# Performance work log

Measured on AMD Instinct MI355X. Metric: run time of the kernel, lower is better.

Reference implementation:

```python
import jax, jax.numpy as jnp
import numpy as np

B, T, F = 2048, 96, 32
H = 1024
G_EMB = 16
LSTM_IN = F + 11 + 1 + G_EMB  # 60


def _lstm_cell(x, h, c, W_ih, W_hh, b):
    g = x @ W_ih.T + h @ W_hh.T + b
    i, f, gg, o = jnp.split(g, 4, axis=-1)  # torch gate order: i, f, g, o
    c_new = jax.nn.sigmoid(f) * c + jax.nn.sigmoid(i) * jnp.tanh(gg)
    h_new = jax.nn.sigmoid(o) * jnp.tanh(c_new)
    return h_new, c_new


def setup_inputs() -> dict:
    key = jax.random.key(0)
    ks = jax.random.split(key, 26)
    s = 1.0 / np.sqrt(H)
    inp = {
        "dec_known": jax.random.normal(ks[0], (B, T, F), jnp.float32),
        "target_y": jax.random.normal(ks[1], (B, T, 1), jnp.float32),
        "enc_h": jax.random.normal(ks[2], (2, B, H), jnp.float32),
        "enc_c": jax.random.normal(ks[3], (2, B, H), jnp.float32),
        "last_enc_consumption": jax.random.normal(ks[4], (B, 1), jnp.float32),
        "group_ids": jax.random.randint(ks[5], (B,), 0, 1000),
        "cat_province": jax.random.randint(ks[6], (B,), 0, 13),
        "cat_customer_type": jax.random.randint(ks[7], (B,), 0, 2),
        "cat_price_type": jax.random.randint(ks[8], (B,), 0, 5),
        "cat_consumption_level": jax.random.randint(ks[9], (B,), 0, 3),
        # learned parameters
        "group_emb": jax.random.normal(ks[10], (1000, G_EMB), jnp.float32),
        "emb_province": jax.random.normal(ks[11], (13, 4), jnp.float32),
        "emb_customer_type": jax.random.normal(ks[12], (2, 2), jnp.float32),
        "emb_price_type": jax.random.normal(ks[13], (5, 3), jnp.float32),
        "emb_consumption_level": jax.random.normal(ks[14], (3, 2), jnp.float32),
        "W_ih0": jax.random.normal(ks[15], (4 * H, LSTM_IN), jnp.float32) * s,
        "W_hh0": jax.random.normal(ks[16], (4 * H, H), jnp.float32) * s,
        "b0": jax.random.normal(ks[17], (4 * H,), jnp.float32) * s,
        "W_ih1": jax.random.normal(ks[18], (4 * H, H), jnp.float32) * s,
        "W_hh1": jax.random.normal(ks[19], (4 * H, H), jnp.float32) * s,
        "b1": jax.random.normal(ks[20], (4 * H,), jnp.float32) * s,
        "W_proj": jax.random.normal(ks[21], (1, H), jnp.float32) * s,
        "b_proj": jnp.zeros((1,), jnp.float32),
    }
    return inp


def reference(dec_known, target_y, enc_h, enc_c, last_enc_consumption,
              group_ids, cat_province, cat_customer_type, cat_price_type,
              cat_consumption_level, group_emb, emb_province, emb_customer_type,
              emb_price_type, emb_consumption_level, W_ih0, W_hh0, b0,
              W_ih1, W_hh1, b1, W_proj, b_proj):
    b, t, _ = dec_known.shape
    # static per-sample features (categorical + group embeddings)
    cat_emb = jnp.concatenate([
        emb_province[cat_province], emb_customer_type[cat_customer_type],
        emb_price_type[cat_price_type], emb_consumption_level[cat_consumption_level],
    ], axis=-1)  # [B, 11]
    group_vec = group_emb[group_ids]  # [B, 16]
    static = jnp.concatenate([cat_emb, group_vec], axis=-1)  # [B, 27]
    # teacher_forcing_ratio = 1.0 => prev_y is last_enc_consumption then target_y shifted
    prev_y = jnp.concatenate([last_enc_consumption[:, None, :], target_y[:, :-1, :]], axis=1)  # [B,T,1]
    x = jnp.concatenate([
        prev_y, dec_known,
        jnp.broadcast_to(static[:, None, :], (b, t, static.shape[-1])),
    ], axis=-1)  # [B, T, 60]

    def step(carry, x_t):
        h1, c1, h2, c2 = carry
        h1, c1 = _lstm_cell(x_t, h1, c1, W_ih0, W_hh0, b0)
        h2, c2 = _lstm_cell(h1, h2, c2, W_ih1, W_hh1, b1)
        return (h1, c1, h2, c2), h2

    init = (enc_h[0], enc_c[0], enc_h[1], enc_c[1])
    _, hs = jax.lax.scan(step, init, jnp.swapaxes(x, 0, 1))  # hs: [T, B, H]
    y = jnp.einsum('tbh,oh->bto', hs, W_proj) + b_proj  # [B, T, 1]
    return y
```

## Files before the change

### kernel.cpp

```cpp
#include <hip/hip_runtime.h>
#include <hip/hip_bf16.h>
#include <stdint.h>


#define BB  2048
#define TT  96
#define NG  4096
#define NT0 34
#define NT1 64

typedef __bf16 bf16;
typedef __bf16 bf16x8 __attribute__((ext_vector_type(8)));
typedef float  f32x4  __attribute__((ext_vector_type(4)));

__device__ __forceinline__ float sigm(float x) { return 1.0f / (1.0f + __expf(-x)); }
__device__ __forceinline__ float ftanh(float x) { return 2.0f / (1.0f + __expf(-2.0f * x)) - 1.0f; }

__device__ __forceinline__ void gload16(const bf16* g, bf16* l) {
  __builtin_amdgcn_global_load_lds((const __attribute__((address_space(1))) void*)g,
                                   (__attribute__((address_space(3))) void*)l, 16, 0, 0);
}

#define SB()  __builtin_amdgcn_sched_barrier(0)
#define BAR() __builtin_amdgcn_s_barrier()


__global__ __launch_bounds__(256) void build_wf1(const float* __restrict__ Wih1,
                                                 const float* __restrict__ Whh1,
                                                 bf16* __restrict__ Wf) {
  int idx = blockIdx.x * 256 + threadIdx.x;
  if (idx >= 32 * NT1 * 4096) return;
  int j = idx & 7, lane = (idx >> 3) & 63, mw = (idx >> 9) & 3;
  int wg = (idx >> 11) & 1, kt = (idx >> 12) & 63, panel = idx >> 18;
  int np = panel * 128 + wg * 64 + mw * 16 + (lane & 15);
  int k  = kt * 32 + ((lane >> 4) << 3) + j;
  int n  = (np & 3) * 1024 + (np >> 2);
  float v = (k < 1024) ? Wih1[n * 1024 + k] : Whh1[n * 1024 + (k - 1024)];
  Wf[idx] = (bf16)v;
}

__global__ __launch_bounds__(256) void build_wf0(const float* __restrict__ Wih0,
                                                 const float* __restrict__ Whh0,
                                                 bf16* __restrict__ Wf) {
  int idx = blockIdx.x * 256 + threadIdx.x;
  if (idx >= 32 * NT0 * 4096) return;
  int j = idx & 7, lane = (idx >> 3) & 63, mw = (idx >> 9) & 3;
  int wg = (idx >> 11) & 1;
  int rem = idx >> 12;
  int kt = rem % NT0, panel = rem / NT0;
  int np = panel * 128 + wg * 64 + mw * 16 + (lane & 15);
  int k  = kt * 32 + ((lane >> 4) << 3) + j;
  int n  = (np & 3) * 1024 + (np >> 2);
  float v;
  if (k < 60)      v = Wih0[n * 60 + k];
  else if (k < 64) v = 0.0f;
  else             v = Whh0[n * 1024 + (k - 64)];
  Wf[idx] = (bf16)v;
}

__global__ __launch_bounds__(256) void perm_bias(const float* __restrict__ b0,
                                                 const float* __restrict__ b1,
                                                 float* __restrict__ b0p,
                                                 float* __restrict__ b1p) {
  int idx = blockIdx.x * 256 + threadIdx.x;
  if (idx >= NG) return;
  int n = (idx & 3) * 1024 + (idx >> 2);
  b0p[idx] = b0[n];
  b1p[idx] = b1[n];
}

__global__ __launch_bounds__(256) void build_x(
    const float* __restrict__ dec, const float* __restrict__ ty, const float* __restrict__ lec,
    const int* __restrict__ gid, const int* __restrict__ cp, const int* __restrict__ cct,
    const int* __restrict__ cpt, const int* __restrict__ ccl,
    const float* __restrict__ gemb, const float* __restrict__ ep, const float* __restrict__ ect,
    const float* __restrict__ ept, const float* __restrict__ ecl,
    bf16* __restrict__ X) {
  int idx = blockIdx.x * 256 + threadIdx.x;
  if (idx >= BB * TT) return;
  int b = idx / TT, t = idx % TT;
  bf16* x = X + (size_t)idx * 64;
  x[0] = (bf16)((t == 0) ? lec[b] : ty[b * TT + t - 1]);
  const float* d = dec + (size_t)idx * 32;
  #pragma unroll
  for (int k = 0; k < 32; ++k) x[1 + k] = (bf16)d[k];
  const float* e;
  e = ep  + cp[b]  * 4;  for (int j = 0; j < 4;  ++j) x[33 + j] = (bf16)e[j];
  e = ect + cct[b] * 2;  for (int j = 0; j < 2;  ++j) x[37 + j] = (bf16)e[j];
  e = ept + cpt[b] * 3;  for (int j = 0; j < 3;  ++j) x[39 + j] = (bf16)e[j];
  e = ecl + ccl[b] * 2;  for (int j = 0; j < 2;  ++j) x[42 + j] = (bf16)e[j];
  e = gemb + gid[b] * 16; for (int j = 0; j < 16; ++j) x[44 + j] = (bf16)e[j];
  for (int j = 60; j < 64; ++j) x[j] = (bf16)0.0f;
}

__global__ __launch_bounds__(256) void init_state(const float* __restrict__ enc_h,
                                                  const float* __restrict__ enc_c,
                                                  bf16* __restrict__ H1b,
                                                  bf16* __restrict__ H2b,
                                                  float* __restrict__ c1t,
                                                  float* __restrict__ c2t) {
  int idx = blockIdx.x * 256 + threadIdx.x;
  if (idx >= BB * 1024) return;
  int b = idx >> 10, h = idx & 1023;
  H1b[idx] = (bf16)enc_h[idx];
  H2b[idx] = (bf16)enc_h[(size_t)BB * 1024 + idx];
  c1t[(size_t)h * BB + b] = enc_c[idx];
  c2t[(size_t)h * BB + b] = enc_c[(size_t)BB * 1024 + idx];
}


template <int MODE>
__device__ __forceinline__ void body(
    int tm, int tn, int t,
    const bf16* __restrict__ P0, const bf16* __restrict__ P1,
    const bf16* __restrict__ Wf, const float* __restrict__ bperm,
    float* __restrict__ ct, bf16* __restrict__ Hout,
    const float* __restrict__ wp, const float* __restrict__ bp,
    float* __restrict__ y, bf16* As)
{
  constexpr int NT = MODE ? NT1 : NT0;

  const int tid = threadIdx.x;
  const int lane = tid & 63, w = tid >> 6;
  const int lrow = lane & 15, u = lane >> 4;
  const int wb = w & 1, wg = w >> 1;

  f32x4 acc[4][4];
  #pragma unroll
  for (int mw = 0; mw < 4; ++mw)
    #pragma unroll
    for (int nb = 0; nb < 4; ++nb) acc[mw][nb] = (f32x4){0.f, 0.f, 0.f, 0.f};

  const int r0 = tid >> 2, r1 = (256 + tid) >> 2;
  const int kc0 = (((tid & 3) ^ ((r0 >> 1) & 3)) << 3);
  const int kc1 = (((tid & 3) ^ ((r1 >> 1) & 3)) << 3);
  const int d0 = (tid & ~63) * 8;
  const int d1 = 2048 + d0;
  const int klocal = ((((lane >> 4) ^ (lrow >> 1)) & 3) << 3);

  auto aptr = [&](int row, int kt, int kc) -> const bf16* {
    if constexpr (MODE == 0) {
      return (kt < 2) ? (P0 + ((size_t)(tm + row) * TT + t) * 64 + kt * 32 + kc)
                      : (P1 + (size_t)(tm + row) * 1024 + (kt - 2) * 32 + kc);
    } else {
      return (kt < 32) ? (P0 + (size_t)(tm + row) * 1024 + kt * 32 + kc)
                       : (P1 + (size_t)(tm + row) * 1024 + (kt - 32) * 32 + kc);
    }
  };
  auto stageA = [&](int kt, bf16* buf) {
    gload16(aptr(r0, kt, kc0), buf + d0);
    gload16(aptr(r1, kt, kc1), buf + d1);
  };

  const bf16* wfbase = Wf + ((size_t)(tn >> 7) * NT) * 4096 + wg * 2048 + lane * 8;
  auto loadW = [&](bf16x8 (&wf)[4], int kt) {
    const bf16* p = wfbase + (size_t)kt * 4096;
    #pragma unroll
    for (int mw = 0; mw < 4; ++mw)
      wf[mw] = *reinterpret_cast<const bf16x8*>(p + mw * 512);
  };

  bf16x8 wfA[4], wfB[4];

  stageA(0, As);
  loadW(wfA, 0);
  stageA(1, As + 4096);
  asm volatile("s_waitcnt vmcnt(2)" ::: "memory");
  SB(); BAR(); SB();

  auto iter = [&](int kt, bf16x8 (&cur)[4], bf16x8 (&nxt)[4]) {
    bf16* buf = As + ((kt & 1) ? 4096 : 0);
    bf16x8 af[4];
    #pragma unroll
    for (int nb = 0; nb < 4; ++nb)
      af[nb] = *reinterpret_cast<const bf16x8*>(&buf[(wb * 64 + nb * 16 + lrow) * 32 + klocal]);
    asm volatile("s_waitcnt lgkmcnt(0)" ::: "memory");
    SB(); BAR(); SB();
    if (kt + 2 < NT) stageA(kt + 2, buf);
    if (kt + 1 < NT) loadW(nxt, kt + 1);
    SB();
    __builtin_amdgcn_s_setprio(1);
    #pragma unroll
    for (int mw = 0; mw < 4; ++mw)
      #pragma unroll
      for (int nb = 0; nb < 4; ++nb)
        acc[mw][nb] = __builtin_amdgcn_mfma_f32_16x16x32_bf16(cur[mw], af[nb], acc[mw][nb], 0, 0, 0);
    __builtin_amdgcn_s_setprio(0);
    if (kt + 2 < NT)      { asm volatile("s_waitcnt vmcnt(6)" ::: "memory"); }
    else if (kt + 1 < NT) { asm volatile("s_waitcnt vmcnt(4)" ::: "memory"); }
    else                  { asm volatile("s_waitcnt vmcnt(0)" ::: "memory"); }
    SB(); BAR(); SB();
  };

  for (int kt = 0; kt < NT; kt += 2) {
    iter(kt,     wfA, wfB);
    iter(kt + 1, wfB, wfA);
  }

  bf16* hst = As + w * 1024;
  const int hq = (tn >> 2) + wg * 16;
  const int bgb = tm + wb * 64;
  float yp[4] = {0.f, 0.f, 0.f, 0.f};

  #pragma unroll
  for (int mw = 0; mw < 4; ++mw) {
    int hg = hq + mw * 4 + u;
    f32x4 bv = *reinterpret_cast<const f32x4*>(&bperm[hg * 4]);
    float wph = 0.f;
    if constexpr (MODE == 1) wph = wp[hg];
    #pragma unroll
    for (int nb = 0; nb < 4; ++nb) {
      int bg = bgb + nb * 16 + lrow;
      float gi = acc[mw][nb][0] + bv[0];
      float gf = acc[mw][nb][1] + bv[1];
      float gg = acc[mw][nb][2] + bv[2];
      float go = acc[mw][nb][3] + bv[3];
      float* cp_ = ct + (size_t)hg * BB + bg;
      float c = *cp_;
      float cn = sigm(gf) * c + sigm(gi) * ftanh(gg);
      float hn = sigm(go) * ftanh(cn);
      *cp_ = cn;
      hst[(nb * 16 + lrow) * 16 + mw * 4 + u] = (bf16)hn;
      if constexpr (MODE == 1) yp[nb] += hn * wph;
    }
  }

  asm volatile("s_waitcnt lgkmcnt(0)" ::: "memory");
  SB();

  #pragma unroll
  for (int q = 0; q < 2; ++q) {
    int chunk = q * 64 + lane;
    int row = chunk >> 1, half = chunk & 1;
    bf16x8 v = *reinterpret_cast<const bf16x8*>(&hst[row * 16 + half * 8]);
    *reinterpret_cast<bf16x8*>(&Hout[(size_t)(bgb + row) * 1024 + hq + half * 8]) = v;
  }

  if constexpr (MODE == 1) {
    #pragma unroll
    for (int nb = 0; nb < 4; ++nb) {
      float s = yp[nb];
      s += __shfl_xor(s, 16);
      s += __shfl_xor(s, 32);
      if (lane < 16)
        atomicAdd(&y[(size_t)(bgb + nb * 16 + lane) * TT + t], s);
    }
  } else {
    if (tn == 0 && tid < 128) y[(size_t)(tm + tid) * TT + t] = bp[0];
  }
}

__global__ __launch_bounds__(256, 3) void step_kernel(
    const bf16* __restrict__ H1in, const bf16* __restrict__ H2in,
    bf16* __restrict__ H1out, bf16* __restrict__ H2out,
    const bf16* __restrict__ X,
    const bf16* __restrict__ Wf0, const bf16* __restrict__ Wf1,
    const float* __restrict__ b0p, const float* __restrict__ b1p,
    float* __restrict__ c1t, float* __restrict__ c2t,
    const float* __restrict__ wp, const float* __restrict__ bp,
    float* __restrict__ y, int t2, int only_l1) {
  __shared__ alignas(16) bf16 As[2 * 4096];
  int bid = (int)blockIdx.x;
  if (only_l1 || bid >= 512) {
    int v = only_l1 ? bid : bid - 512;
    int t1 = t2 + 1;
    if (t1 >= TT) return;
    int x = v & 7, j = v >> 3;
    int tm  = (j & 15) << 7;
    int tn0 = ((x << 1) + (j >> 4)) << 8;
    body<0>(tm, tn0, t1, X, H1in, Wf0, b0p, c1t, H1out, nullptr, bp, y, As);
    __syncthreads();
    body<0>(tm, tn0 + 128, t1, X, H1in, Wf0, b0p, c1t, H1out, nullptr, bp, y, As);
  } else {
    int x = bid & 7, j = bid >> 3;
    int tm = (j & 15) << 7;
    int tn = ((x << 2) + (j >> 4)) << 7;
    body<1>(tm, tn, t2, H1in, H2in, Wf1, b1p, c2t, H2out, wp, nullptr, y, As);
  }
}


extern "C" void kernel_launch(void* const* d_in, const int* in_sizes, int n_in,
                              void* d_out, int out_size, void* d_ws, size_t ws_size,
                              hipStream_t stream) {
  const float* dec   = (const float*)d_in[0];
  const float* ty    = (const float*)d_in[1];
  const float* enc_h = (const float*)d_in[2];
  const float* enc_c = (const float*)d_in[3];
  const float* lec   = (const float*)d_in[4];
  const int*   gid   = (const int*)d_in[5];
  const int*   cp    = (const int*)d_in[6];
  const int*   cct   = (const int*)d_in[7];
  const int*   cpt   = (const int*)d_in[8];
  const int*   ccl   = (const int*)d_in[9];
  const float* gemb  = (const float*)d_in[10];
  const float* ep    = (const float*)d_in[11];
  const float* ect   = (const float*)d_in[12];
  const float* ept   = (const float*)d_in[13];
  const float* ecl   = (const float*)d_in[14];
  const float* Wih0  = (const float*)d_in[15];
  const float* Whh0  = (const float*)d_in[16];
  const float* b0    = (const float*)d_in[17];
  const float* Wih1  = (const float*)d_in[18];
  const float* Whh1  = (const float*)d_in[19];
  const float* b1    = (const float*)d_in[20];
  const float* wp    = (const float*)d_in[21];
  const float* bp    = (const float*)d_in[22];
  float* y = (float*)d_out;

  char* ws = (char*)d_ws;
  bf16* Wf1   = (bf16*)ws;  ws += (size_t)32 * NT1 * 4096 * 2;
  bf16* Wf0   = (bf16*)ws;  ws += (size_t)32 * NT0 * 4096 * 2;
  bf16* X     = (bf16*)ws;  ws += (size_t)BB * TT * 64 * 2;
  bf16* H1a   = (bf16*)ws;  ws += (size_t)BB * 1024 * 2;
  bf16* H1b   = (bf16*)ws;  ws += (size_t)BB * 1024 * 2;
  bf16* H2a   = (bf16*)ws;  ws += (size_t)BB * 1024 * 2;
  bf16* H2b   = (bf16*)ws;  ws += (size_t)BB * 1024 * 2;
  float* c1t  = (float*)ws; ws += (size_t)BB * 1024 * 4;
  float* c2t  = (float*)ws; ws += (size_t)BB * 1024 * 4;
  float* b0p  = (float*)ws; ws += (size_t)NG * 4;
  float* b1p  = (float*)ws; ws += (size_t)NG * 4;

  build_wf1<<<(32 * NT1 * 4096) / 256, 256, 0, stream>>>(Wih1, Whh1, Wf1);
  build_wf0<<<(32 * NT0 * 4096 + 255) / 256, 256, 0, stream>>>(Wih0, Whh0, Wf0);
  perm_bias<<<NG / 256, 256, 0, stream>>>(b0, b1, b0p, b1p);
  build_x<<<(BB * TT + 255) / 256, 256, 0, stream>>>(dec, ty, lec, gid, cp, cct, cpt, ccl,
                                                     gemb, ep, ect, ept, ecl, X);
  init_state<<<(BB * 1024) / 256, 256, 0, stream>>>(enc_h, enc_c, H1b, H2b, c1t, c2t);

  step_kernel<<<256, 256, 0, stream>>>(H1b, nullptr, H1a, nullptr, X, Wf0, Wf1,
                                       b0p, b1p, c1t, c2t, wp, bp, y, -1, 1);
  for (int t = 0; t < TT; ++t) {
    bf16* h1i = (t & 1) ? H1b : H1a;
    bf16* h1o = (t & 1) ? H1a : H1b;
    bf16* h2i = (t & 1) ? H2a : H2b;
    bf16* h2o = (t & 1) ? H2b : H2a;
    step_kernel<<<768, 256, 0, stream>>>(h1i, h2i, h1o, h2o, X, Wf0, Wf1,
                                         b0p, b1p, c1t, c2t, wp, bp, y, t, 0);
  }
}
```

Measured before the change: 6.973 ms.

## Widen gate tile to 256 columns per block, halving step grid

Each block now computes a 128x256 output tile (8 gate fragments per wave instead of 4), and the weight panel layout is rebuilt to match. Layer-0 blocks no longer loop over two 128-wide halves, and layer-1 blocks each cover 256 columns, so each step launches 512 blocks instead of 768. Every activation tile loaded into LDS now feeds twice as many MFMAs, which cuts A-operand traffic and barrier overhead per FLOP. The cost is twice the accumulator and weight registers, with launch bounds lowered to 2 blocks per CU, so fewer blocks and waves are available to hide latency.

```diff
diff --git a/kernel.cpp b/kernel.cpp
--- a/kernel.cpp
+++ b/kernel.cpp
@@ -29,10 +29,10 @@
                                                  const float* __restrict__ Whh1,
                                                  bf16* __restrict__ Wf) {
   int idx = blockIdx.x * 256 + threadIdx.x;
-  if (idx >= 32 * NT1 * 4096) return;
-  int j = idx & 7, lane = (idx >> 3) & 63, mw = (idx >> 9) & 3;
-  int wg = (idx >> 11) & 1, kt = (idx >> 12) & 63, panel = idx >> 18;
-  int np = panel * 128 + wg * 64 + mw * 16 + (lane & 15);
+  if (idx >= 16 * NT1 * 8192) return;
+  int j = idx & 7, lane = (idx >> 3) & 63, gf = (idx >> 9) & 7;
+  int wg = (idx >> 12) & 1, kt = (idx >> 13) & 63, panel = idx >> 19;
+  int np = panel * 256 + wg * 128 + gf * 16 + (lane & 15);
   int k  = kt * 32 + ((lane >> 4) << 3) + j;
   int n  = (np & 3) * 1024 + (np >> 2);
   float v = (k < 1024) ? Wih1[n * 1024 + k] : Whh1[n * 1024 + (k - 1024)];
@@ -43,12 +43,12 @@
                                                  const float* __restrict__ Whh0,
                                                  bf16* __restrict__ Wf) {
   int idx = blockIdx.x * 256 + threadIdx.x;
-  if (idx >= 32 * NT0 * 4096) return;
-  int j = idx & 7, lane = (idx >> 3) & 63, mw = (idx >> 9) & 3;
-  int wg = (idx >> 11) & 1;
-  int rem = idx >> 12;
+  if (idx >= 16 * NT0 * 8192) return;
+  int j = idx & 7, lane = (idx >> 3) & 63, gf = (idx >> 9) & 7;
+  int wg = (idx >> 12) & 1;
+  int rem = idx >> 13;
   int kt = rem % NT0, panel = rem / NT0;
-  int np = panel * 128 + wg * 64 + mw * 16 + (lane & 15);
+  int np = panel * 256 + wg * 128 + gf * 16 + (lane & 15);
   int k  = kt * 32 + ((lane >> 4) << 3) + j;
   int n  = (np & 3) * 1024 + (np >> 2);
   float v;
@@ -125,11 +125,11 @@
   const int lrow = lane & 15, u = lane >> 4;
   const int wb = w & 1, wg = w >> 1;
 
-  f32x4 acc[4][4];
+  f32x4 acc[8][4];
   #pragma unroll
-  for (int mw = 0; mw < 4; ++mw)
-    #pragma unroll
-    for (int nb = 0; nb < 4; ++nb) acc[mw][nb] = (f32x4){0.f, 0.f, 0.f, 0.f};
+  for (int gf = 0; gf < 8; ++gf)
+    #pragma unroll
+    for (int bf = 0; bf < 4; ++bf) acc[gf][bf] = (f32x4){0.f, 0.f, 0.f, 0.f};
 
   const int r0 = tid >> 2, r1 = (256 + tid) >> 2;
   const int kc0 = (((tid & 3) ^ ((r0 >> 1) & 3)) << 3);
@@ -152,28 +152,28 @@
     gload16(aptr(r1, kt, kc1), buf + d1);
   };
 
-  const bf16* wfbase = Wf + ((size_t)(tn >> 7) * NT) * 4096 + wg * 2048 + lane * 8;
-  auto loadW = [&](bf16x8 (&wf)[4], int kt) {
-    const bf16* p = wfbase + (size_t)kt * 4096;
-    #pragma unroll
-    for (int mw = 0; mw < 4; ++mw)
-      wf[mw] = *reinterpret_cast<const bf16x8*>(p + mw * 512);
+  const bf16* wfbase = Wf + (size_t)(tn >> 8) * NT * 8192 + wg * 4096 + lane * 8;
+  auto loadW = [&](bf16x8 (&wf)[8], int kt) {
+    const bf16* p = wfbase + (size_t)kt * 8192;
+    #pragma unroll
+    for (int gf = 0; gf < 8; ++gf)
+      wf[gf] = *reinterpret_cast<const bf16x8*>(p + gf * 512);
   };
 
-  bf16x8 wfA[4], wfB[4];
+  bf16x8 wfA[8], wfB[8];
 
   stageA(0, As);
   loadW(wfA, 0);
   stageA(1, As + 4096);
-  asm volatile("s_waitcnt vmcnt(2)" ::: "memory");
+  asm volatile("s_waitcnt vmcnt(10)" ::: "memory");
   SB(); BAR(); SB();
 
-  auto iter = [&](int kt, bf16x8 (&cur)[4], bf16x8 (&nxt)[4]) {
+  auto iter = [&](int kt, bf16x8 (&cur)[8], bf16x8 (&nxt)[8]) {
     bf16* buf = As + ((kt & 1) ? 4096 : 0);
     bf16x8 af[4];
     #pragma unroll
-    for (int nb = 0; nb < 4; ++nb)
-      af[nb] = *reinterpret_cast<const bf16x8*>(&buf[(wb * 64 + nb * 16 + lrow) * 32 + klocal]);
+    for (int bf = 0; bf < 4; ++bf)
+      af[bf] = *reinterpret_cast<const bf16x8*>(&buf[(wb * 64 + bf * 16 + lrow) * 32 + klocal]);
     asm volatile("s_waitcnt lgkmcnt(0)" ::: "memory");
     SB(); BAR(); SB();
     if (kt + 2 < NT) stageA(kt + 2, buf);
@@ -181,13 +181,13 @@
     SB();
     __builtin_amdgcn_s_setprio(1);
     #pragma unroll
-    for (int mw = 0; mw < 4; ++mw)
+    for (int gf = 0; gf < 8; ++gf)
       #pragma unroll
-      for (int nb = 0; nb < 4; ++nb)
-        acc[mw][nb] = __builtin_amdgcn_mfma_f32_16x16x32_bf16(cur[mw], af[nb], acc[mw][nb], 0, 0, 0);
+      for (int bf = 0; bf < 4; ++bf)
+        acc[gf][bf] = __builtin_amdgcn_mfma_f32_16x16x32_bf16(cur[gf], af[bf], acc[gf][bf], 0, 0, 0);
     __builtin_amdgcn_s_setprio(0);
-    if (kt + 2 < NT)      { asm volatile("s_waitcnt vmcnt(6)" ::: "memory"); }
-    else if (kt + 1 < NT) { asm volatile("s_waitcnt vmcnt(4)" ::: "memory"); }
+    if (kt + 2 < NT)      { asm volatile("s_waitcnt vmcnt(10)" ::: "memory"); }
+    else if (kt + 1 < NT) { asm volatile("s_waitcnt vmcnt(8)" ::: "memory"); }
     else                  { asm volatile("s_waitcnt vmcnt(0)" ::: "memory"); }
     SB(); BAR(); SB();
   };
@@ -197,31 +197,31 @@
     iter(kt + 1, wfB, wfA);
   }
 
-  bf16* hst = As + w * 1024;
-  const int hq = (tn >> 2) + wg * 16;
+  bf16* hst = As + w * 2048;
+  const int hq = (tn >> 2) + wg * 32;
   const int bgb = tm + wb * 64;
   float yp[4] = {0.f, 0.f, 0.f, 0.f};
 
   #pragma unroll
-  for (int mw = 0; mw < 4; ++mw) {
-    int hg = hq + mw * 4 + u;
+  for (int gf = 0; gf < 8; ++gf) {
+    int hg = hq + gf * 4 + u;
     f32x4 bv = *reinterpret_cast<const f32x4*>(&bperm[hg * 4]);
     float wph = 0.f;
     if constexpr (MODE == 1) wph = wp[hg];
     #pragma unroll
-    for (int nb = 0; nb < 4; ++nb) {
-      int bg = bgb + nb * 16 + lrow;
-      float gi = acc[mw][nb][0] + bv[0];
-      float gf = acc[mw][nb][1] + bv[1];
-      float gg = acc[mw][nb][2] + bv[2];
-      float go = acc[mw][nb][3] + bv[3];
+    for (int bf = 0; bf < 4; ++bf) {
+      int bg = bgb + bf * 16 + lrow;
+      float gi = acc[gf][bf][0] + bv[0];
+      float gf_ = acc[gf][bf][1] + bv[1];
+      float gg = acc[gf][bf][2] + bv[2];
+      float go = acc[gf][bf][3] + bv[3];
       float* cp_ = ct + (size_t)hg * BB + bg;
       float c = *cp_;
-      float cn = sigm(gf) * c + sigm(gi) * ftanh(gg);
+      float cn = sigm(gf_) * c + sigm(gi) * ftanh(gg);
       float hn = sigm(go) * ftanh(cn);
       *cp_ = cn;
-      hst[(nb * 16 + lrow) * 16 + mw * 4 + u] = (bf16)hn;
-      if constexpr (MODE == 1) yp[nb] += hn * wph;
+      hst[(bf * 16 + lrow) * 32 + gf * 4 + u] = (bf16)hn;
+      if constexpr (MODE == 1) yp[bf] += hn * wph;
     }
   }
 
@@ -229,28 +229,28 @@
   SB();
 
   #pragma unroll
-  for (int q = 0; q < 2; ++q) {
+  for (int q = 0; q < 4; ++q) {
     int chunk = q * 64 + lane;
-    int row = chunk >> 1, half = chunk & 1;
-    bf16x8 v = *reinterpret_cast<const bf16x8*>(&hst[row * 16 + half * 8]);
-    *reinterpret_cast<bf16x8*>(&Hout[(size_t)(bgb + row) * 1024 + hq + half * 8]) = v;
+    int row = chunk >> 2, seg = chunk & 3;
+    bf16x8 v = *reinterpret_cast<const bf16x8*>(&hst[row * 32 + seg * 8]);
+    *reinterpret_cast<bf16x8*>(&Hout[(size_t)(bgb + row) * 1024 + hq + seg * 8]) = v;
   }
 
   if constexpr (MODE == 1) {
     #pragma unroll
-    for (int nb = 0; nb < 4; ++nb) {
-      float s = yp[nb];
+    for (int bf = 0; bf < 4; ++bf) {
+      float s = yp[bf];
       s += __shfl_xor(s, 16);
       s += __shfl_xor(s, 32);
       if (lane < 16)
-        atomicAdd(&y[(size_t)(bgb + nb * 16 + lane) * TT + t], s);
+        atomicAdd(&y[(size_t)(bgb + bf * 16 + lane) * TT + t], s);
     }
   } else {
     if (tn == 0 && tid < 128) y[(size_t)(tm + tid) * TT + t] = bp[0];
   }
 }
 
-__global__ __launch_bounds__(256, 3) void step_kernel(
+__global__ __launch_bounds__(256, 2) void step_kernel(
     const bf16* __restrict__ H1in, const bf16* __restrict__ H2in,
     bf16* __restrict__ H1out, bf16* __restrict__ H2out,
     const bf16* __restrict__ X,
@@ -261,20 +261,18 @@
     float* __restrict__ y, int t2, int only_l1) {
   __shared__ alignas(16) bf16 As[2 * 4096];
   int bid = (int)blockIdx.x;
-  if (only_l1 || bid >= 512) {
-    int v = only_l1 ? bid : bid - 512;
+  if (only_l1 || bid >= 256) {
+    int v = only_l1 ? bid : bid - 256;
     int t1 = t2 + 1;
     if (t1 >= TT) return;
-    int x = v & 7, j = v >> 3;
-    int tm  = (j & 15) << 7;
-    int tn0 = ((x << 1) + (j >> 4)) << 8;
-    body<0>(tm, tn0, t1, X, H1in, Wf0, b0p, c1t, H1out, nullptr, bp, y, As);
-    __syncthreads();
-    body<0>(tm, tn0 + 128, t1, X, H1in, Wf0, b0p, c1t, H1out, nullptr, bp, y, As);
+    int x = v & 7, r = v >> 3;
+    int tm = (r & 15) << 7;
+    int tn = ((x << 1) + (r >> 4)) << 8;
+    body<0>(tm, tn, t1, X, H1in, Wf0, b0p, c1t, H1out, nullptr, bp, y, As);
   } else {
-    int x = bid & 7, j = bid >> 3;
-    int tm = (j & 15) << 7;
-    int tn = ((x << 2) + (j >> 4)) << 7;
+    int x = bid & 7, r = bid >> 3;
+    int tm = (r & 15) << 7;
+    int tn = ((x << 1) + (r >> 4)) << 8;
     body<1>(tm, tn, t2, H1in, H2in, Wf1, b1p, c2t, H2out, wp, nullptr, y, As);
   }
 }
@@ -309,8 +307,8 @@
   float* y = (float*)d_out;
 
   char* ws = (char*)d_ws;
-  bf16* Wf1   = (bf16*)ws;  ws += (size_t)32 * NT1 * 4096 * 2;
-  bf16* Wf0   = (bf16*)ws;  ws += (size_t)32 * NT0 * 4096 * 2;
+  bf16* Wf1   = (bf16*)ws;  ws += (size_t)16 * NT1 * 8192 * 2;
+  bf16* Wf0   = (bf16*)ws;  ws += (size_t)16 * NT0 * 8192 * 2;
   bf16* X     = (bf16*)ws;  ws += (size_t)BB * TT * 64 * 2;
   bf16* H1a   = (bf16*)ws;  ws += (size_t)BB * 1024 * 2;
   bf16* H1b   = (bf16*)ws;  ws += (size_t)BB * 1024 * 2;
@@ -321,8 +319,8 @@
   float* b0p  = (float*)ws; ws += (size_t)NG * 4;
   float* b1p  = (float*)ws; ws += (size_t)NG * 4;
 
-  build_wf1<<<(32 * NT1 * 4096) / 256, 256, 0, stream>>>(Wih1, Whh1, Wf1);
-  build_wf0<<<(32 * NT0 * 4096 + 255) / 256, 256, 0, stream>>>(Wih0, Whh0, Wf0);
+  build_wf1<<<(16 * NT1 * 8192) / 256, 256, 0, stream>>>(Wih1, Whh1, Wf1);
+  build_wf0<<<(16 * NT0 * 8192 + 255) / 256, 256, 0, stream>>>(Wih0, Whh0, Wf0);
   perm_bias<<<NG / 256, 256, 0, stream>>>(b0, b1, b0p, b1p);
   build_x<<<(BB * TT + 255) / 256, 256, 0, stream>>>(dec, ty, lec, gid, cp, cct, cpt, ccl,
                                                      gemb, ep, ect, ept, ecl, X);
@@ -335,7 +333,7 @@
     bf16* h1o = (t & 1) ? H1a : H1b;
     bf16* h2i = (t & 1) ? H2a : H2b;
     bf16* h2o = (t & 1) ? H2b : H2a;
-    step_kernel<<<768, 256, 0, stream>>>(h1i, h2i, h1o, h2o, X, Wf0, Wf1,
+    step_kernel<<<512, 256, 0, stream>>>(h1i, h2i, h1o, h2o, X, Wf0, Wf1,
                                          b0p, b1p, c1t, c2t, wp, bp, y, t, 0);
   }
 }
```

Result: faster. 6.392 ms (-8.3%).
